# Kernel tuning notes

Hardware: AMD Instinct MI355X
Metric: run time of the kernel (lower is better)

## Reference

```python
import jax, jax.numpy as jnp
import numpy as np

CHUNK = 64  # chunk_size
EPS = 1e-6


def setup_inputs() -> dict:
    key = jax.random.key(0)
    ks = jax.random.split(key, 7)
    b, L, H, dh, ds = 2, 4096, 16, 64, 64
    X = jax.random.normal(ks[0], (b, L, H, dh), dtype=jnp.float32)
    # negative log-decay in (-1, 0) for numerical stability (Mamba2 convention)
    A = -jax.random.uniform(ks[1], (b, L, H), dtype=jnp.float32)
    B = jax.random.normal(ks[2], (b, L, H, ds), dtype=jnp.float32)
    C = jax.random.normal(ks[3], (b, L, H, ds), dtype=jnp.float32)
    log2_alpha_base = jnp.full((H,), -0.15, dtype=jnp.float32) + 0.02 * jax.random.normal(ks[4], (H,), dtype=jnp.float32)
    log2_beta = 0.02 * jax.random.normal(ks[5], (H,), dtype=jnp.float32)
    surprise_ema = jnp.ones((H,), dtype=jnp.float32)
    return {"X": X, "A": A, "B": B, "C": C,
            "log2_alpha_base": log2_alpha_base, "log2_beta": log2_beta,
            "surprise_ema": surprise_ema}


def reference(X, A, B, C, log2_alpha_base, log2_beta, surprise_ema):
    b, L, H, dh = X.shape
    ds = B.shape[-1]
    n = L // CHUNK  # L is a multiple of CHUNK (no padding needed)

    # [b, h, n, c, ...] layout
    Xt = X.reshape(b, n, CHUNK, H, dh).transpose(0, 3, 1, 2, 4)   # b h n c dh
    At = A.reshape(b, n, CHUNK, H).transpose(0, 3, 1, 2)          # b h n c
    Bt = B.reshape(b, n, CHUNK, H, ds).transpose(0, 3, 1, 2, 4)   # b h n c ds
    Ct = C.reshape(b, n, CHUNK, H, ds).transpose(0, 3, 1, 2, 4)   # b h n c ds

    # per-chunk surprise from outer-product state delta
    BX = jnp.einsum('bhncs,bhncd->bhnsd', Bt, Xt)                 # b h n ds dh
    chunk_surprise = (BX ** 2).mean(axis=(-1, -2))                # b h n

    # surprise gate (eval mode: EMA buffer not updated)
    normalized = chunk_surprise / (surprise_ema[None, :, None] + EPS)
    log2c = jnp.clip(log2_alpha_base, -3.32, -0.015)
    alpha_base = 1.0 - jnp.exp2(log2c)                            # [H]
    beta = jnp.exp2(jnp.clip(log2_beta, -2.0, 2.0))               # [H]
    boost = jax.nn.relu(jnp.tanh(beta[None, :, None] * normalized))
    alpha = jnp.clip(alpha_base[None, :, None]
                     + (1.0 - alpha_base[None, :, None]) * boost, 0.01, 0.999)

    # surprise-modulated decay
    A_mod = At * (1.0 - alpha)[..., None]                         # b h n c
    A_cs = jnp.cumsum(A_mod, axis=-1)                             # b h n c

    # intra-chunk attention-like term with causal decay matrix
    diff = A_cs[..., :, None] - A_cs[..., None, :]                # b h n c c
    causal = jnp.tril(jnp.ones((CHUNK, CHUNK), dtype=bool))
    Lmat = jnp.where(causal, jnp.exp(diff), 0.0)
    CB = jnp.einsum('bhnid,bhnjd->bhnij', Ct, Bt)
    Y_intra = jnp.einsum('bhnij,bhnjd->bhnid', Lmat * CB, Xt)

    # inter-chunk state carry (sequential over chunks)
    decay_chunk = jnp.exp(A_mod.sum(axis=-1))                     # b h n
    decay_to_end = jnp.exp(A_cs[..., -1:] - A_cs)                 # b h n c
    h_final = jnp.einsum('bhnc,bhncs,bhncd->bhnsd', decay_to_end, Bt, Xt)

    def step(carry, inp):
        dc, hf = inp                                              # dc: b h ; hf: b h ds dh
        return dc[..., None, None] * carry + hf, carry

    dc_n = jnp.moveaxis(decay_chunk, 2, 0)                        # n b h
    hf_n = jnp.moveaxis(h_final, 2, 0)                            # n b h ds dh
    init = jnp.zeros((b, H, ds, dh), X.dtype)
    _, h_inter_n = jax.lax.scan(step, init, (dc_n, hf_n))
    h_inter = jnp.moveaxis(h_inter_n, 0, 2)                       # b h n ds dh

    decay_from_start = jnp.exp(A_cs)
    Y_inter = jnp.einsum('bhnis,bhnsp,bhni->bhnip', Ct, h_inter, decay_from_start)

    Y = (Y_intra + Y_inter).transpose(0, 2, 3, 1, 4).reshape(b, L, H, dh)
    return Y
```

## Files before the change

### kernel.cpp

```cpp
#include <hip/hip_runtime.h>
#include <hip/hip_bf16.h>
#include <math.h>

#define LSEQ 4096
#define NH   16
#define DH   64
#define CH   64
#define NCH  64

typedef __attribute__((ext_vector_type(8))) short bf16x8;
typedef __attribute__((ext_vector_type(4))) short s16x4;
typedef __attribute__((ext_vector_type(4))) float f32x4;

#define MFMA16(a, b, c) __builtin_amdgcn_mfma_f32_16x16x32_bf16((a), (b), (c), 0, 0, 0)

__device__ __forceinline__ int swz(int row, int col) {
    return (row << 6) + (col ^ ((row & 7) << 3));
}

__device__ __forceinline__ float4 ld4(const float* p) {
    return *reinterpret_cast<const float4*>(p);
}
__device__ __forceinline__ short f2b(float x) {
    __hip_bfloat16 h = __float2bfloat16(x);
    return *reinterpret_cast<short*>(&h);
}
__device__ __forceinline__ float b2f(short s) {
    union { unsigned u; float f; } v;
    v.u = ((unsigned)(unsigned short)s) << 16;
    return v.f;
}
__device__ __forceinline__ s16x4 pack4(float a, float b, float c, float d) {
    s16x4 r; r.x = f2b(a); r.y = f2b(b); r.z = f2b(c); r.w = f2b(d); return r;
}
__device__ __forceinline__ uint2 sx2(uint2 v, int m) {
    uint2 r;
    r.x = (unsigned)__shfl_xor((int)v.x, m, 64);
    r.y = (unsigned)__shfl_xor((int)v.y, m, 64);
    return r;
}
__device__ __forceinline__ short ext4(uint2 u, int g) {
    unsigned word = (g & 2) ? u.y : u.x;
    return (short)((g & 1) ? (word >> 16) : (word & 0xffffu));
}

__global__ __launch_bounds__(256) void ssd_k1(
    const float* __restrict__ X, const float* __restrict__ A,
    const float* __restrict__ B, const float* __restrict__ C,
    const float* __restrict__ l2ab, const float* __restrict__ l2b,
    const float* __restrict__ ema,
    unsigned short* __restrict__ yw, unsigned short* __restrict__ hf,
    float* __restrict__ dcb, float* __restrict__ dfs)
{
    __shared__ __align__(16) short R1[CH * 64];
    __shared__ __align__(16) short R2[CH * 64];
    __shared__ __align__(16) short R3[CH * 64];
    __shared__ __align__(16) float red[4];

    const int tid  = threadIdx.x;
    const int blk  = blockIdx.x;
    const int nidx = blk & (NCH - 1);
    const int h    = (blk >> 6) & (NH - 1);
    const int bb   = blk >> 10;
    const size_t base = ((size_t)(bb * LSEQ + nidx * CH) * NH + h) * DH;

    const int lane = tid & 63;
    const int w    = tid >> 6;
    const int rb   = 16 * w;
    const int fr   = lane & 15;
    const int gq   = lane >> 4;
    const int g4   = 4 * gq;
    const int ko   = 8 * gq;
    const int rot  = (fr >> 1) & 3;

    const int sc = tid >> 4, sd0 = (tid & 15) * 4;

    #pragma unroll
    for (int m = 0; m < 4; ++m) {
        int c = sc + 16 * m;
        size_t g = base + (size_t)c * 1024 + sd0;
        float4 xv = ld4(&X[g]);
        float4 bv = ld4(&B[g]);
        float4 cv = ld4(&C[g]);
        *reinterpret_cast<s16x4*>(&R1[swz(c, sd0)]) = pack4(xv.x, xv.y, xv.z, xv.w);
        *reinterpret_cast<s16x4*>(&R2[swz(c, sd0)]) = pack4(bv.x, bv.y, bv.z, bv.w);
        *reinterpret_cast<s16x4*>(&R3[swz(c, sd0)]) = pack4(cv.x, cv.y, cv.z, cv.w);
    }
    float aval = A[(size_t)(bb * LSEQ + nidx * CH + lane) * NH + h];
    __syncthreads();

    float cum = aval;
    #pragma unroll
    for (int off = 1; off < 64; off <<= 1) {
        float t = __shfl_up(cum, off, 64);
        if (lane >= off) cum += t;
    }
    float cum_tot = __shfl(cum, 63, 64);

    const f32x4 zf = {0.f, 0.f, 0.f, 0.f};

    bf16x8 aX0 = *reinterpret_cast<const bf16x8*>(&R1[swz(rb + fr, 0  + ko)]);
    bf16x8 aX1 = *reinterpret_cast<const bf16x8*>(&R1[swz(rb + fr, 32 + ko)]);
    bf16x8 aB0 = *reinterpret_cast<const bf16x8*>(&R2[swz(rb + fr, 0  + ko)]);
    bf16x8 aB1 = *reinterpret_cast<const bf16x8*>(&R2[swz(rb + fr, 32 + ko)]);
    bf16x8 aC0 = *reinterpret_cast<const bf16x8*>(&R3[swz(rb + fr, 0  + ko)]);
    bf16x8 aC1 = *reinterpret_cast<const bf16x8*>(&R3[swz(rb + fr, 32 + ko)]);
    f32x4 aCB[4];
    float ss = 0.f;
    #pragma unroll
    for (int n = 0; n < 4; ++n) {
        bf16x8 bX0 = *reinterpret_cast<const bf16x8*>(&R1[swz(16 * n + fr, 0  + ko)]);
        bf16x8 bX1 = *reinterpret_cast<const bf16x8*>(&R1[swz(16 * n + fr, 32 + ko)]);
        bf16x8 bB0 = *reinterpret_cast<const bf16x8*>(&R2[swz(16 * n + fr, 0  + ko)]);
        bf16x8 bB1 = *reinterpret_cast<const bf16x8*>(&R2[swz(16 * n + fr, 32 + ko)]);
        f32x4 gx = MFMA16(aX1, bX1, MFMA16(aX0, bX0, zf));
        f32x4 gb = MFMA16(aB1, bB1, MFMA16(aB0, bB0, zf));
        aCB[n]   = MFMA16(aC1, bB1, MFMA16(aC0, bB0, zf));
        #pragma unroll
        for (int r = 0; r < 4; ++r) ss = fmaf(gx[r], gb[r], ss);
    }
    #pragma unroll
    for (int off = 32; off > 0; off >>= 1) ss += __shfl_down(ss, off, 64);
    if (lane == 0) red[w] = ss;
    __syncthreads();

    float4 rv = *reinterpret_cast<const float4*>(red);
    float surprise = (rv.x + rv.y + rv.z + rv.w) * (1.f / 4096.f);
    float l2c   = fminf(fmaxf(l2ab[h], -3.32f), -0.015f);
    float ab_   = 1.f - exp2f(l2c);
    float bt    = exp2f(fminf(fmaxf(l2b[h], -2.f), 2.f));
    float nrm   = surprise / (ema[h] + 1e-6f);
    float boost = fmaxf(tanhf(bt * nrm), 0.f);
    float alpha = fminf(fmaxf(ab_ + (1.f - ab_) * boost, 0.01f), 0.999f);
    float scale = 1.f - alpha;
    float v    = cum * scale;
    float tot  = cum_tot * scale;
    float epv  = __expf(v);
    float env  = __expf(-v);
    float dtev = __expf(tot - v);
    if (w == 0) {
        dfs[(size_t)blk * CH + lane] = epv;
        if (lane == 63) dcb[blk] = __expf(tot);
    }

    {
        float epi[4], enj[4];
        #pragma unroll
        for (int r = 0; r < 4; ++r) epi[r] = __shfl(epv, rb + g4 + r, 64);
        #pragma unroll
        for (int n = 0; n < 4; ++n) enj[n] = __shfl(env, 16 * n + fr, 64);
        #pragma unroll
        for (int n = 0; n < 4; ++n)
            #pragma unroll
            for (int r = 0; r < 4; ++r) {
                int i = rb + g4 + r, j = 16 * n + fr;
                float val = (j <= i) ? epi[r] * enj[n] * aCB[n][r] : 0.f;
                R3[swz(i, j)] = f2b(val);
            }
    }

    s16x4 outX[4], outB[4];
    const int d0 = 4 * fr;
    #pragma unroll
    for (int m = 0; m < 4; ++m) {
        int c0 = 16 * w + 4 * ((m + rot) & 3);
        uint2 mx = *reinterpret_cast<const uint2*>(&R1[swz(c0 + gq, d0)]);
        uint2 mb = *reinterpret_cast<const uint2*>(&R2[swz(c0 + gq, d0)]);
        uint2 px_ = sx2(mx, 16), pb_ = sx2(mb, 16);
        uint2 xe = (gq & 1) ? px_ : mx, xo = (gq & 1) ? mx : px_;
        uint2 be = (gq & 1) ? pb_ : mb, bo = (gq & 1) ? mb : pb_;
        uint2 xpe = sx2(xe, 32), xpo = sx2(xo, 32);
        uint2 bpe = sx2(be, 32), bpo = sx2(bo, 32);
        uint2 xr0 = (gq & 2) ? xpe : xe, xr1 = (gq & 2) ? xpo : xo;
        uint2 xr2 = (gq & 2) ? xe : xpe, xr3 = (gq & 2) ? xo : xpo;
        uint2 br0 = (gq & 2) ? bpe : be, br1 = (gq & 2) ? bpo : bo;
        uint2 br2 = (gq & 2) ? be : bpe, br3 = (gq & 2) ? bo : bpo;
        s16x4 ox; ox.x = ext4(xr0, gq); ox.y = ext4(xr1, gq);
                  ox.z = ext4(xr2, gq); ox.w = ext4(xr3, gq);
        outX[m] = ox;
        float dt0 = __shfl(dtev, c0 + 0, 64), dt1 = __shfl(dtev, c0 + 1, 64);
        float dt2 = __shfl(dtev, c0 + 2, 64), dt3 = __shfl(dtev, c0 + 3, 64);
        s16x4 ob;
        ob.x = f2b(b2f(ext4(br0, gq)) * dt0);
        ob.y = f2b(b2f(ext4(br1, gq)) * dt1);
        ob.z = f2b(b2f(ext4(br2, gq)) * dt2);
        ob.w = f2b(b2f(ext4(br3, gq)) * dt3);
        outB[m] = ob;
    }
    __syncthreads();

    #pragma unroll
    for (int m = 0; m < 4; ++m) {
        int c0 = 16 * w + 4 * ((m + rot) & 3);
        *reinterpret_cast<s16x4*>(&R1[swz(d0 + gq, c0)]) = outX[m];
        *reinterpret_cast<s16x4*>(&R2[swz(d0 + gq, c0)]) = outB[m];
    }
    __syncthreads();

    __builtin_amdgcn_s_setprio(1);
    f32x4 acc2[4] = {zf, zf, zf, zf};
    f32x4 acc3[4] = {zf, zf, zf, zf};
    #pragma unroll
    for (int k0 = 0; k0 < 64; k0 += 32) {
        bf16x8 aX = *reinterpret_cast<const bf16x8*>(&R1[swz(rb + fr, k0 + ko)]);
        bf16x8 aB = *reinterpret_cast<const bf16x8*>(&R2[swz(rb + fr, k0 + ko)]);
        #pragma unroll
        for (int n = 0; n < 4; ++n) {
            bf16x8 bT = *reinterpret_cast<const bf16x8*>(&R3[swz(16 * n + fr, k0 + ko)]);
            bf16x8 bX = *reinterpret_cast<const bf16x8*>(&R1[swz(16 * n + fr, k0 + ko)]);
            acc2[n] = MFMA16(aX, bT, acc2[n]);
            acc3[n] = MFMA16(aB, bX, acc3[n]);
        }
    }
    __builtin_amdgcn_s_setprio(0);
    #pragma unroll
    for (int n = 0; n < 4; ++n) {
        int colI = 16 * n + fr;
        s16x4 y4 = pack4(acc2[n][0], acc2[n][1], acc2[n][2], acc2[n][3]);
        s16x4 h4 = pack4(acc3[n][0], acc3[n][1], acc3[n][2], acc3[n][3]);
        *reinterpret_cast<s16x4*>(&yw[(size_t)blk * 4096 + colI * 64 + rb + g4]) = y4;
        *reinterpret_cast<s16x4*>(&hf[(size_t)blk * 4096 + colI * 64 + rb + g4]) = h4;
    }
}

__global__ __launch_bounds__(256) void ssd_k2(
    unsigned int* __restrict__ hfU, const float* __restrict__ dcb)
{
    __shared__ float sdc[NCH];
    const int tid = threadIdx.x;
    const int bh  = blockIdx.x >> 3;
    const int sub = blockIdx.x & 7;
    if (tid < NCH) sdc[tid] = dcb[bh * NCH + tid];
    __syncthreads();
    const size_t base = (size_t)bh * NCH * 2048 + sub * 256 + tid;

    float c0 = 0.f, c1 = 0.f;
    unsigned int cur[8];
    #pragma unroll
    for (int kk = 0; kk < 8; ++kk) cur[kk] = hfU[base + (size_t)kk * 2048];
    #pragma unroll
    for (int kb = 0; kb < 8; ++kb) {
        unsigned int nxt[8];
        if (kb < 7) {
            #pragma unroll
            for (int kk = 0; kk < 8; ++kk)
                nxt[kk] = hfU[base + (size_t)(8 * kb + 8 + kk) * 2048];
        }
        #pragma unroll
        for (int kk = 0; kk < 8; ++kk) {
            int k = 8 * kb + kk;
            unsigned int u = cur[kk];
            union { unsigned int q; float f; } lo, hi;
            lo.q = u << 16;
            hi.q = u & 0xffff0000u;
            unsigned int packed = (unsigned int)(unsigned short)f2b(c0)
                                | ((unsigned int)(unsigned short)f2b(c1) << 16);
            hfU[base + (size_t)k * 2048] = packed;
            float d = sdc[k];
            c0 = fmaf(d, c0, lo.f);
            c1 = fmaf(d, c1, hi.f);
        }
        if (kb < 7) {
            #pragma unroll
            for (int kk = 0; kk < 8; ++kk) cur[kk] = nxt[kk];
        }
    }
}

__global__ __launch_bounds__(256) void ssd_k3(
    const float* __restrict__ C, const unsigned short* __restrict__ hI,
    const unsigned short* __restrict__ yw, const float* __restrict__ dfs,
    float* __restrict__ Y)
{
    __shared__ __align__(16) short sHt[CH * 64];
    __shared__ __align__(16) short sC2[CH * 64];
    __shared__ float sF[CH];

    const int tid  = threadIdx.x;
    const int blk  = blockIdx.x;
    const int nidx = blk & (NCH - 1);
    const int h    = (blk >> 6) & (NH - 1);
    const int bb   = blk >> 10;
    const size_t base = ((size_t)(bb * LSEQ + nidx * CH) * NH + h) * DH;

    #pragma unroll
    for (int m = 0; m < 2; ++m) {
        int idx = tid + 256 * m;
        int row = idx >> 3, c8 = (idx & 7) * 8;
        bf16x8 v = *reinterpret_cast<const bf16x8*>(&hI[(size_t)blk * 4096 + row * 64 + c8]);
        *reinterpret_cast<bf16x8*>(&sHt[swz(row, c8)]) = v;
    }
    #pragma unroll
    for (int m = 0; m < 4; ++m) {
        int p = tid + 256 * m;
        int row = p >> 4, d0 = (p & 15) * 4;
        float4 cv = ld4(&C[base + (size_t)row * 1024 + d0]);
        *reinterpret_cast<s16x4*>(&sC2[swz(row, d0)]) = pack4(cv.x, cv.y, cv.z, cv.w);
    }
    if (tid < CH) sF[tid] = dfs[(size_t)blk * CH + tid];
    __syncthreads();

    const int lane = tid & 63;
    const int w    = tid >> 6;
    const int rb   = 16 * w;
    const int fr   = lane & 15;
    const int g4   = 4 * (lane >> 4);
    const int ko   = 8 * (lane >> 4);
    const f32x4 zf = {0.f, 0.f, 0.f, 0.f};

    __builtin_amdgcn_s_setprio(1);
    f32x4 acc[4] = {zf, zf, zf, zf};
    #pragma unroll
    for (int k0 = 0; k0 < 64; k0 += 32) {
        bf16x8 a = *reinterpret_cast<const bf16x8*>(&sHt[swz(rb + fr, k0 + ko)]);
        #pragma unroll
        for (int n = 0; n < 4; ++n) {
            bf16x8 b = *reinterpret_cast<const bf16x8*>(&sC2[swz(16 * n + fr, k0 + ko)]);
            acc[n] = MFMA16(a, b, acc[n]);
        }
    }
    __builtin_amdgcn_s_setprio(0);
    #pragma unroll
    for (int n = 0; n < 4; ++n) {
        int i  = 16 * n + fr;
        int p0 = rb + g4;
        float f = sF[i];
        s16x4 y4 = *reinterpret_cast<const s16x4*>(&yw[(size_t)blk * 4096 + i * 64 + p0]);
        float4 o;
        o.x = fmaf(f, acc[n][0], b2f(y4.x));
        o.y = fmaf(f, acc[n][1], b2f(y4.y));
        o.z = fmaf(f, acc[n][2], b2f(y4.z));
        o.w = fmaf(f, acc[n][3], b2f(y4.w));
        *reinterpret_cast<float4*>(&Y[base + (size_t)i * 1024 + p0]) = o;
    }
}

extern "C" void kernel_launch(void* const* d_in, const int* in_sizes, int n_in,
                              void* d_out, int out_size, void* d_ws, size_t ws_size,
                              hipStream_t stream)
{
    const float* X    = (const float*)d_in[0];
    const float* A    = (const float*)d_in[1];
    const float* B    = (const float*)d_in[2];
    const float* C    = (const float*)d_in[3];
    const float* l2ab = (const float*)d_in[4];
    const float* l2b  = (const float*)d_in[5];
    const float* ema  = (const float*)d_in[6];
    float* Y = (float*)d_out;

    unsigned short* hf = (unsigned short*)d_ws;
    unsigned short* yw = hf + (size_t)8388608;
    float* dcb = (float*)(yw + (size_t)8388608);
    float* dfs = dcb + 2048;

    const int nblk = 2 * NH * NCH;
    ssd_k1<<<nblk, 256, 0, stream>>>(X, A, B, C, l2ab, l2b, ema, yw, hf, dcb, dfs);
    ssd_k2<<<256, 256, 0, stream>>>((unsigned int*)hf, dcb);
    ssd_k3<<<nblk, 256, 0, stream>>>(C, hf, yw, dfs, Y);
}
```

Measured before the change: 57.67 us.

## Process two heads per block in ssd_k1 for wider contiguous loads

```diff
diff --git a/kernel.cpp b/kernel.cpp
--- a/kernel.cpp
+++ b/kernel.cpp
@@ -52,17 +52,18 @@
     unsigned short* __restrict__ yw, unsigned short* __restrict__ hf,
     float* __restrict__ dcb, float* __restrict__ dfs)
 {
-    __shared__ __align__(16) short R1[CH * 64];
-    __shared__ __align__(16) short R2[CH * 64];
-    __shared__ __align__(16) short R3[CH * 64];
-    __shared__ __align__(16) float red[4];
+    __shared__ __align__(16) short R1[2][CH * 64];
+    __shared__ __align__(16) short R2[2][CH * 64];
+    __shared__ __align__(16) short R3[2][CH * 64];
+    __shared__ __align__(16) float red[2][4];
 
     const int tid  = threadIdx.x;
     const int blk  = blockIdx.x;
-    const int nidx = blk & (NCH - 1);
-    const int h    = (blk >> 6) & (NH - 1);
-    const int bb   = blk >> 10;
-    const size_t base = ((size_t)(bb * LSEQ + nidx * CH) * NH + h) * DH;
+    const int nidx = blk & 63;
+    const int hp   = (blk >> 6) & 7;
+    const int bb   = blk >> 9;
+    const int h0   = hp * 2;
+    const size_t base2 = ((size_t)(bb * LSEQ + nidx * CH)) * 1024 + hp * 128;
 
     const int lane = tid & 63;
     const int w    = tid >> 6;
@@ -73,153 +74,177 @@
     const int ko   = 8 * gq;
     const int rot  = (fr >> 1) & 3;
 
-    const int sc = tid >> 4, sd0 = (tid & 15) * 4;
-
-    #pragma unroll
-    for (int m = 0; m < 4; ++m) {
-        int c = sc + 16 * m;
-        size_t g = base + (size_t)c * 1024 + sd0;
+    #pragma unroll
+    for (int m = 0; m < 8; ++m) {
+        int p = tid + 256 * m;
+        int c = p >> 5;
+        int q = p & 31;
+        int e = q >> 4;
+        int dd = (q & 15) * 4;
+        size_t g = base2 + (size_t)c * 1024 + q * 4;
         float4 xv = ld4(&X[g]);
         float4 bv = ld4(&B[g]);
         float4 cv = ld4(&C[g]);
-        *reinterpret_cast<s16x4*>(&R1[swz(c, sd0)]) = pack4(xv.x, xv.y, xv.z, xv.w);
-        *reinterpret_cast<s16x4*>(&R2[swz(c, sd0)]) = pack4(bv.x, bv.y, bv.z, bv.w);
-        *reinterpret_cast<s16x4*>(&R3[swz(c, sd0)]) = pack4(cv.x, cv.y, cv.z, cv.w);
-    }
-    float aval = A[(size_t)(bb * LSEQ + nidx * CH + lane) * NH + h];
-    __syncthreads();
-
-    float cum = aval;
+        *reinterpret_cast<s16x4*>(&R1[e][swz(c, dd)]) = pack4(xv.x, xv.y, xv.z, xv.w);
+        *reinterpret_cast<s16x4*>(&R2[e][swz(c, dd)]) = pack4(bv.x, bv.y, bv.z, bv.w);
+        *reinterpret_cast<s16x4*>(&R3[e][swz(c, dd)]) = pack4(cv.x, cv.y, cv.z, cv.w);
+    }
+    float av0 = A[((size_t)(bb * LSEQ + nidx * CH + lane)) * NH + h0];
+    float av1 = A[((size_t)(bb * LSEQ + nidx * CH + lane)) * NH + h0 + 1];
+    __syncthreads();
+
+    float cum0 = av0, cum1 = av1;
     #pragma unroll
     for (int off = 1; off < 64; off <<= 1) {
-        float t = __shfl_up(cum, off, 64);
-        if (lane >= off) cum += t;
-    }
-    float cum_tot = __shfl(cum, 63, 64);
+        float t0 = __shfl_up(cum0, off, 64);
+        float t1 = __shfl_up(cum1, off, 64);
+        if (lane >= off) { cum0 += t0; cum1 += t1; }
+    }
+    float ctot0 = __shfl(cum0, 63, 64);
+    float ctot1 = __shfl(cum1, 63, 64);
 
     const f32x4 zf = {0.f, 0.f, 0.f, 0.f};
 
-    bf16x8 aX0 = *reinterpret_cast<const bf16x8*>(&R1[swz(rb + fr, 0  + ko)]);
-    bf16x8 aX1 = *reinterpret_cast<const bf16x8*>(&R1[swz(rb + fr, 32 + ko)]);
-    bf16x8 aB0 = *reinterpret_cast<const bf16x8*>(&R2[swz(rb + fr, 0  + ko)]);
-    bf16x8 aB1 = *reinterpret_cast<const bf16x8*>(&R2[swz(rb + fr, 32 + ko)]);
-    bf16x8 aC0 = *reinterpret_cast<const bf16x8*>(&R3[swz(rb + fr, 0  + ko)]);
-    bf16x8 aC1 = *reinterpret_cast<const bf16x8*>(&R3[swz(rb + fr, 32 + ko)]);
-    f32x4 aCB[4];
-    float ss = 0.f;
-    #pragma unroll
-    for (int n = 0; n < 4; ++n) {
-        bf16x8 bX0 = *reinterpret_cast<const bf16x8*>(&R1[swz(16 * n + fr, 0  + ko)]);
-        bf16x8 bX1 = *reinterpret_cast<const bf16x8*>(&R1[swz(16 * n + fr, 32 + ko)]);
-        bf16x8 bB0 = *reinterpret_cast<const bf16x8*>(&R2[swz(16 * n + fr, 0  + ko)]);
-        bf16x8 bB1 = *reinterpret_cast<const bf16x8*>(&R2[swz(16 * n + fr, 32 + ko)]);
-        f32x4 gx = MFMA16(aX1, bX1, MFMA16(aX0, bX0, zf));
-        f32x4 gb = MFMA16(aB1, bB1, MFMA16(aB0, bB0, zf));
-        aCB[n]   = MFMA16(aC1, bB1, MFMA16(aC0, bB0, zf));
-        #pragma unroll
-        for (int r = 0; r < 4; ++r) ss = fmaf(gx[r], gb[r], ss);
-    }
-    #pragma unroll
-    for (int off = 32; off > 0; off >>= 1) ss += __shfl_down(ss, off, 64);
-    if (lane == 0) red[w] = ss;
-    __syncthreads();
-
-    float4 rv = *reinterpret_cast<const float4*>(red);
-    float surprise = (rv.x + rv.y + rv.z + rv.w) * (1.f / 4096.f);
-    float l2c   = fminf(fmaxf(l2ab[h], -3.32f), -0.015f);
-    float ab_   = 1.f - exp2f(l2c);
-    float bt    = exp2f(fminf(fmaxf(l2b[h], -2.f), 2.f));
-    float nrm   = surprise / (ema[h] + 1e-6f);
-    float boost = fmaxf(tanhf(bt * nrm), 0.f);
-    float alpha = fminf(fmaxf(ab_ + (1.f - ab_) * boost, 0.01f), 0.999f);
-    float scale = 1.f - alpha;
-    float v    = cum * scale;
-    float tot  = cum_tot * scale;
-    float epv  = __expf(v);
-    float env  = __expf(-v);
-    float dtev = __expf(tot - v);
-    if (w == 0) {
-        dfs[(size_t)blk * CH + lane] = epv;
-        if (lane == 63) dcb[blk] = __expf(tot);
-    }
-
-    {
-        float epi[4], enj[4];
-        #pragma unroll
-        for (int r = 0; r < 4; ++r) epi[r] = __shfl(epv, rb + g4 + r, 64);
-        #pragma unroll
-        for (int n = 0; n < 4; ++n) enj[n] = __shfl(env, 16 * n + fr, 64);
-        #pragma unroll
-        for (int n = 0; n < 4; ++n)
-            #pragma unroll
-            for (int r = 0; r < 4; ++r) {
-                int i = rb + g4 + r, j = 16 * n + fr;
-                float val = (j <= i) ? epi[r] * enj[n] * aCB[n][r] : 0.f;
-                R3[swz(i, j)] = f2b(val);
+    f32x4 aCB[2][4];
+    #pragma unroll
+    for (int e = 0; e < 2; ++e) {
+        bf16x8 aX0 = *reinterpret_cast<const bf16x8*>(&R1[e][swz(rb + fr, 0  + ko)]);
+        bf16x8 aX1 = *reinterpret_cast<const bf16x8*>(&R1[e][swz(rb + fr, 32 + ko)]);
+        bf16x8 aB0 = *reinterpret_cast<const bf16x8*>(&R2[e][swz(rb + fr, 0  + ko)]);
+        bf16x8 aB1 = *reinterpret_cast<const bf16x8*>(&R2[e][swz(rb + fr, 32 + ko)]);
+        bf16x8 aC0 = *reinterpret_cast<const bf16x8*>(&R3[e][swz(rb + fr, 0  + ko)]);
+        bf16x8 aC1 = *reinterpret_cast<const bf16x8*>(&R3[e][swz(rb + fr, 32 + ko)]);
+        float ss = 0.f;
+        #pragma unroll
+        for (int n = 0; n < 4; ++n) {
+            bf16x8 bX0 = *reinterpret_cast<const bf16x8*>(&R1[e][swz(16 * n + fr, 0  + ko)]);
+            bf16x8 bX1 = *reinterpret_cast<const bf16x8*>(&R1[e][swz(16 * n + fr, 32 + ko)]);
+            bf16x8 bB0 = *reinterpret_cast<const bf16x8*>(&R2[e][swz(16 * n + fr, 0  + ko)]);
+            bf16x8 bB1 = *reinterpret_cast<const bf16x8*>(&R2[e][swz(16 * n + fr, 32 + ko)]);
+            f32x4 gx = MFMA16(aX1, bX1, MFMA16(aX0, bX0, zf));
+            f32x4 gb = MFMA16(aB1, bB1, MFMA16(aB0, bB0, zf));
+            aCB[e][n] = MFMA16(aC1, bB1, MFMA16(aC0, bB0, zf));
+            #pragma unroll
+            for (int r = 0; r < 4; ++r) ss = fmaf(gx[r], gb[r], ss);
+        }
+        #pragma unroll
+        for (int off = 32; off > 0; off >>= 1) ss += __shfl_down(ss, off, 64);
+        if (lane == 0) red[e][w] = ss;
+    }
+    __syncthreads();
+
+    s16x4 outX[2][4], outB[2][4];
+    const int d0 = 4 * fr;
+    float epvA[2], envA[2], dtevA[2];
+    #pragma unroll
+    for (int e = 0; e < 2; ++e) {
+        const int h = h0 + e;
+        const int gblk = ((bb * NH + h) << 6) | nidx;
+        float cum  = e ? cum1 : cum0;
+        float ctot = e ? ctot1 : ctot0;
+
+        float4 rv = *reinterpret_cast<const float4*>(red[e]);
+        float surprise = (rv.x + rv.y + rv.z + rv.w) * (1.f / 4096.f);
+        float l2c   = fminf(fmaxf(l2ab[h], -3.32f), -0.015f);
+        float ab_   = 1.f - exp2f(l2c);
+        float bt    = exp2f(fminf(fmaxf(l2b[h], -2.f), 2.f));
+        float nrm   = surprise / (ema[h] + 1e-6f);
+        float boost = fmaxf(tanhf(bt * nrm), 0.f);
+        float alpha = fminf(fmaxf(ab_ + (1.f - ab_) * boost, 0.01f), 0.999f);
+        float scale = 1.f - alpha;
+        float v    = cum * scale;
+        float tot  = ctot * scale;
+        float epv  = __expf(v);
+        float env  = __expf(-v);
+        float dtev = __expf(tot - v);
+        epvA[e] = epv; envA[e] = env; dtevA[e] = dtev;
+        if (w == 0) {
+            dfs[(size_t)gblk * CH + lane] = epv;
+            if (lane == 63) dcb[gblk] = __expf(tot);
+        }
+
+        {
+            float epi[4], enj[4];
+            #pragma unroll
+            for (int r = 0; r < 4; ++r) epi[r] = __shfl(epv, rb + g4 + r, 64);
+            #pragma unroll
+            for (int n = 0; n < 4; ++n) enj[n] = __shfl(env, 16 * n + fr, 64);
+            #pragma unroll
+            for (int n = 0; n < 4; ++n)
+                #pragma unroll
+                for (int r = 0; r < 4; ++r) {
+                    int i = rb + g4 + r, j = 16 * n + fr;
+                    float val = (j <= i) ? epi[r] * enj[n] * aCB[e][n][r] : 0.f;
+                    R3[e][swz(i, j)] = f2b(val);
+                }
+        }
+
+        #pragma unroll
+        for (int m = 0; m < 4; ++m) {
+            int c0 = 16 * w + 4 * ((m + rot) & 3);
+            uint2 mx = *reinterpret_cast<const uint2*>(&R1[e][swz(c0 + gq, d0)]);
+            uint2 mb = *reinterpret_cast<const uint2*>(&R2[e][swz(c0 + gq, d0)]);
+            uint2 px_ = sx2(mx, 16), pb_ = sx2(mb, 16);
+            uint2 xe = (gq & 1) ? px_ : mx, xo = (gq & 1) ? mx : px_;
+            uint2 be = (gq & 1) ? pb_ : mb, bo = (gq & 1) ? mb : pb_;
+            uint2 xpe = sx2(xe, 32), xpo = sx2(xo, 32);
+            uint2 bpe = sx2(be, 32), bpo = sx2(bo, 32);
+            uint2 xr0 = (gq & 2) ? xpe : xe, xr1 = (gq & 2) ? xpo : xo;
+            uint2 xr2 = (gq & 2) ? xe : xpe, xr3 = (gq & 2) ? xo : xpo;
+            uint2 br0 = (gq & 2) ? bpe : be, br1 = (gq & 2) ? bpo : bo;
+            uint2 br2 = (gq & 2) ? be : bpe, br3 = (gq & 2) ? bo : bpo;
+            s16x4 ox; ox.x = ext4(xr0, gq); ox.y = ext4(xr1, gq);
+                      ox.z = ext4(xr2, gq); ox.w = ext4(xr3, gq);
+            outX[e][m] = ox;
+            float dt0 = __shfl(dtev, c0 + 0, 64), dt1 = __shfl(dtev, c0 + 1, 64);
+            float dt2 = __shfl(dtev, c0 + 2, 64), dt3 = __shfl(dtev, c0 + 3, 64);
+            s16x4 ob;
+            ob.x = f2b(b2f(ext4(br0, gq)) * dt0);
+            ob.y = f2b(b2f(ext4(br1, gq)) * dt1);
+            ob.z = f2b(b2f(ext4(br2, gq)) * dt2);
+            ob.w = f2b(b2f(ext4(br3, gq)) * dt3);
+            outB[e][m] = ob;
+        }
+    }
+    __syncthreads();
+
+    #pragma unroll
+    for (int e = 0; e < 2; ++e)
+        #pragma unroll
+        for (int m = 0; m < 4; ++m) {
+            int c0 = 16 * w + 4 * ((m + rot) & 3);
+            *reinterpret_cast<s16x4*>(&R1[e][swz(d0 + gq, c0)]) = outX[e][m];
+            *reinterpret_cast<s16x4*>(&R2[e][swz(d0 + gq, c0)]) = outB[e][m];
+        }
+    __syncthreads();
+
+    #pragma unroll
+    for (int e = 0; e < 2; ++e) {
+        const int gblk = ((bb * NH + h0 + e) << 6) | nidx;
+        __builtin_amdgcn_s_setprio(1);
+        f32x4 acc2[4] = {zf, zf, zf, zf};
+        f32x4 acc3[4] = {zf, zf, zf, zf};
+        #pragma unroll
+        for (int k0 = 0; k0 < 64; k0 += 32) {
+            bf16x8 aX = *reinterpret_cast<const bf16x8*>(&R1[e][swz(rb + fr, k0 + ko)]);
+            bf16x8 aB = *reinterpret_cast<const bf16x8*>(&R2[e][swz(rb + fr, k0 + ko)]);
+            #pragma unroll
+            for (int n = 0; n < 4; ++n) {
+                bf16x8 bT = *reinterpret_cast<const bf16x8*>(&R3[e][swz(16 * n + fr, k0 + ko)]);
+                bf16x8 bX = *reinterpret_cast<const bf16x8*>(&R1[e][swz(16 * n + fr, k0 + ko)]);
+                acc2[n] = MFMA16(aX, bT, acc2[n]);
+                acc3[n] = MFMA16(aB, bX, acc3[n]);
             }
-    }
-
-    s16x4 outX[4], outB[4];
-    const int d0 = 4 * fr;
-    #pragma unroll
-    for (int m = 0; m < 4; ++m) {
-        int c0 = 16 * w + 4 * ((m + rot) & 3);
-        uint2 mx = *reinterpret_cast<const uint2*>(&R1[swz(c0 + gq, d0)]);
-        uint2 mb = *reinterpret_cast<const uint2*>(&R2[swz(c0 + gq, d0)]);
-        uint2 px_ = sx2(mx, 16), pb_ = sx2(mb, 16);
-        uint2 xe = (gq & 1) ? px_ : mx, xo = (gq & 1) ? mx : px_;
-        uint2 be = (gq & 1) ? pb_ : mb, bo = (gq & 1) ? mb : pb_;
-        uint2 xpe = sx2(xe, 32), xpo = sx2(xo, 32);
-        uint2 bpe = sx2(be, 32), bpo = sx2(bo, 32);
-        uint2 xr0 = (gq & 2) ? xpe : xe, xr1 = (gq & 2) ? xpo : xo;
-        uint2 xr2 = (gq & 2) ? xe : xpe, xr3 = (gq & 2) ? xo : xpo;
-        uint2 br0 = (gq & 2) ? bpe : be, br1 = (gq & 2) ? bpo : bo;
-        uint2 br2 = (gq & 2) ? be : bpe, br3 = (gq & 2) ? bo : bpo;
-        s16x4 ox; ox.x = ext4(xr0, gq); ox.y = ext4(xr1, gq);
-                  ox.z = ext4(xr2, gq); ox.w = ext4(xr3, gq);
-        outX[m] = ox;
-        float dt0 = __shfl(dtev, c0 + 0, 64), dt1 = __shfl(dtev, c0 + 1, 64);
-        float dt2 = __shfl(dtev, c0 + 2, 64), dt3 = __shfl(dtev, c0 + 3, 64);
-        s16x4 ob;
-        ob.x = f2b(b2f(ext4(br0, gq)) * dt0);
-        ob.y = f2b(b2f(ext4(br1, gq)) * dt1);
-        ob.z = f2b(b2f(ext4(br2, gq)) * dt2);
-        ob.w = f2b(b2f(ext4(br3, gq)) * dt3);
-        outB[m] = ob;
-    }
-    __syncthreads();
-
-    #pragma unroll
-    for (int m = 0; m < 4; ++m) {
-        int c0 = 16 * w + 4 * ((m + rot) & 3);
-        *reinterpret_cast<s16x4*>(&R1[swz(d0 + gq, c0)]) = outX[m];
-        *reinterpret_cast<s16x4*>(&R2[swz(d0 + gq, c0)]) = outB[m];
-    }
-    __syncthreads();
-
-    __builtin_amdgcn_s_setprio(1);
-    f32x4 acc2[4] = {zf, zf, zf, zf};
-    f32x4 acc3[4] = {zf, zf, zf, zf};
-    #pragma unroll
-    for (int k0 = 0; k0 < 64; k0 += 32) {
-        bf16x8 aX = *reinterpret_cast<const bf16x8*>(&R1[swz(rb + fr, k0 + ko)]);
-        bf16x8 aB = *reinterpret_cast<const bf16x8*>(&R2[swz(rb + fr, k0 + ko)]);
+        }
+        __builtin_amdgcn_s_setprio(0);
         #pragma unroll
         for (int n = 0; n < 4; ++n) {
-            bf16x8 bT = *reinterpret_cast<const bf16x8*>(&R3[swz(16 * n + fr, k0 + ko)]);
-            bf16x8 bX = *reinterpret_cast<const bf16x8*>(&R1[swz(16 * n + fr, k0 + ko)]);
-            acc2[n] = MFMA16(aX, bT, acc2[n]);
-            acc3[n] = MFMA16(aB, bX, acc3[n]);
-        }
-    }
-    __builtin_amdgcn_s_setprio(0);
-    #pragma unroll
-    for (int n = 0; n < 4; ++n) {
-        int colI = 16 * n + fr;
-        s16x4 y4 = pack4(acc2[n][0], acc2[n][1], acc2[n][2], acc2[n][3]);
-        s16x4 h4 = pack4(acc3[n][0], acc3[n][1], acc3[n][2], acc3[n][3]);
-        *reinterpret_cast<s16x4*>(&yw[(size_t)blk * 4096 + colI * 64 + rb + g4]) = y4;
-        *reinterpret_cast<s16x4*>(&hf[(size_t)blk * 4096 + colI * 64 + rb + g4]) = h4;
+            int colI = 16 * n + fr;
+            s16x4 y4 = pack4(acc2[n][0], acc2[n][1], acc2[n][2], acc2[n][3]);
+            s16x4 h4 = pack4(acc3[n][0], acc3[n][1], acc3[n][2], acc3[n][3]);
+            *reinterpret_cast<s16x4*>(&yw[(size_t)gblk * 4096 + colI * 64 + rb + g4]) = y4;
+            *reinterpret_cast<s16x4*>(&hf[(size_t)gblk * 4096 + colI * 64 + rb + g4]) = h4;
+        }
     }
 }
 
@@ -353,8 +378,7 @@
     float* dcb = (float*)(yw + (size_t)8388608);
     float* dfs = dcb + 2048;
 
-    const int nblk = 2 * NH * NCH;
-    ssd_k1<<<nblk, 256, 0, stream>>>(X, A, B, C, l2ab, l2b, ema, yw, hf, dcb, dfs);
+    ssd_k1<<<1024, 256, 0, stream>>>(X, A, B, C, l2ab, l2b, ema, yw, hf, dcb, dfs);
     ssd_k2<<<256, 256, 0, stream>>>((unsigned int*)hf, dcb);
-    ssd_k3<<<nblk, 256, 0, stream>>>(C, hf, yw, dfs, Y);
-}
+    ssd_k3<<<2048, 256, 0, stream>>>(C, hf, yw, dfs, Y);
+}
```

New measurement: 65.24 us. 1.13x slower.
